# Optimization experiments

Measured on AMD Instinct MI355X. Metric: run time of the kernel, lower is better.

## Reference

```python
import jax, jax.numpy as jnp
import numpy as np

EPS = 1e-5  # torch BatchNorm default

def _conv(x, w, pad):
    return jax.lax.conv_general_dilated(x, w, window_strides=(1, 1), padding=pad,
                                        dimension_numbers=('NCHW', 'OIHW', 'NCHW'))

def _bn(x, g, b, m, v):
    # eval-mode BatchNorm2d over channel axis 1 of NCHW
    scale = g / jnp.sqrt(v + EPS)
    return x * scale[None, :, None, None] + (b - m * scale)[None, :, None, None]

def _bn1d(x, g, b, m, v):
    scale = g / jnp.sqrt(v + EPS)
    return x * scale[None, :] + (b - m * scale)[None, :]

def _prelu(x, a):
    # torch PReLU with num_parameters=1 (scalar slope, init 0.25)
    return jnp.where(x >= 0, x, a * x)

def setup_inputs():
    key = jax.random.key(0)
    ks = jax.random.split(key, 10)
    B, H, W = 256, 600, 19
    C1, C2 = 40, 40
    x = jax.random.normal(ks[0], (B, H, W), jnp.float32)
    w1 = jax.random.normal(ks[1], (C1, 1, 29, 1), jnp.float32) * 0.1
    w2 = jax.random.normal(ks[2], (C2, C1, 1, 19), jnp.float32) * 0.1
    fc1_w = jax.random.uniform(ks[3], (80, 1560), jnp.float32, -0.005, 0.005)
    fc2_w = jax.random.uniform(ks[4], (2, 80), jnp.float32, -0.005, 0.005)
    def bn_params(k, n):
        k1, k2 = jax.random.split(k)
        return (jnp.ones((n,), jnp.float32), jnp.zeros((n,), jnp.float32),
                jax.random.normal(k1, (n,), jnp.float32) * 0.1,
                jax.random.uniform(k2, (n,), jnp.float32, 0.5, 1.5))
    bn1_g, bn1_b, bn1_m, bn1_v = bn_params(ks[5], C1)
    bn2_g, bn2_b, bn2_m, bn2_v = bn_params(ks[6], C2)
    bn3_g, bn3_b, bn3_m, bn3_v = bn_params(ks[7], 80)
    a1 = jnp.full((1,), 0.25, jnp.float32)
    a2 = jnp.full((1,), 0.25, jnp.float32)
    a3 = jnp.full((1,), 0.25, jnp.float32)
    return dict(x=x, w1=w1, bn1_g=bn1_g, bn1_b=bn1_b, bn1_m=bn1_m, bn1_v=bn1_v, a1=a1,
                w2=w2, bn2_g=bn2_g, bn2_b=bn2_b, bn2_m=bn2_m, bn2_v=bn2_v, a2=a2,
                fc1_w=fc1_w, bn3_g=bn3_g, bn3_b=bn3_b, bn3_m=bn3_m, bn3_v=bn3_v, a3=a3,
                fc2_w=fc2_w)

def reference(x, w1, bn1_g, bn1_b, bn1_m, bn1_v, a1,
              w2, bn2_g, bn2_b, bn2_m, bn2_v, a2,
              fc1_w, bn3_g, bn3_b, bn3_m, bn3_v, a3, fc2_w):
    h = x[:, None, :, :]                                  # [B,1,600,19]
    # conv1: inputs NOT binarized, weights sign-binarized
    h = _conv(h, jnp.sign(w1), [(14, 14), (0, 0)])         # [B,40,600,19]
    h = _prelu(_bn(h, bn1_g, bn1_b, bn1_m, bn1_v), a1)
    # conv2: inputs and weights binarized
    h = _conv(jnp.sign(h), jnp.sign(w2), [(0, 0), (0, 0)])  # [B,40,600,1]
    h = _prelu(_bn(h, bn2_g, bn2_b, bn2_m, bn2_v), a2)
    # AvgPool2d kernel (30,1) stride (15,1)
    h = jax.lax.reduce_window(h, 0.0, jax.lax.add, (1, 1, 30, 1), (1, 1, 15, 1), 'VALID') / 30.0  # [B,40,39,1]
    h = h.reshape(h.shape[0], -1)                          # [B,1560]
    # fc1: binarized input/weight; BatchNorm1d; PReLU; dropout is identity in eval
    h = jnp.sign(h) @ jnp.sign(fc1_w).T                    # [B,80]
    h = _prelu(_bn1d(h, bn3_g, bn3_b, bn3_m, bn3_v), a3)
    out = jnp.sign(h) @ jnp.sign(fc2_w).T                  # [B,2]
    return out
```

## Files before the change

kernel.cpp:

```cpp
#include <hip/hip_runtime.h>
#include <stdint.h>

#define B_ 256
#define H_ 600
#define W_ 19
#define C1_ 40
#define C2_ 40
#define KH_ 29
#define PAD_ 14
#define NW_ 760
#define NWORDS_ 12
#define NJ_ 39
#define FIN_ 1560
#define FOUT_ 80
#define FCW_ 25
#define HS1 150
#define XSTL 179

__device__ __forceinline__ float fsgn(float x){ return (x > 0.f) ? 1.f : ((x < 0.f) ? -1.f : 0.f); }
__device__ __forceinline__ int8_t isgn(float x){ return (int8_t)((x > 0.f) - (x < 0.f)); }

__global__ void k0_setup(const float* __restrict__ w1, const float* __restrict__ w2,
                         const float* __restrict__ fc1w, const float* __restrict__ fc2w,
                         const float* __restrict__ g1, const float* __restrict__ b1,
                         const float* __restrict__ m1, const float* __restrict__ v1,
                         const float* __restrict__ g2, const float* __restrict__ b2,
                         const float* __restrict__ m2, const float* __restrict__ v2,
                         const float* __restrict__ g3, const float* __restrict__ b3,
                         const float* __restrict__ m3, const float* __restrict__ v3,
                         float* __restrict__ w1s, uint64_t* __restrict__ w2m,
                         uint64_t* __restrict__ fc1p, int8_t* __restrict__ fc2s,
                         float* __restrict__ bnp)
{
  int tid = blockIdx.x * blockDim.x + threadIdx.x;
  int np  = gridDim.x * blockDim.x;
  int lane = threadIdx.x & 63;
  int gw   = tid >> 6;
  int nw   = np >> 6;

  for (int i = tid; i < C1_*KH_; i += np) w1s[i] = fsgn(w1[i]);

  for (int v = gw; v < C2_*NWORDS_; v += nw){
    int c2 = v / NWORDS_, wd = v % NWORDS_;
    int idx = wd*64 + lane;
    float val = 0.f;
    if (idx < NW_){
      int c1 = idx % 40, w = idx / 40;
      val = w2[c2*NW_ + c1*W_ + w];
    }
    unsigned long long m = __ballot(val > 0.f);
    if (lane == 0) w2m[c2*NWORDS_ + wd] = m;
  }
  for (int v = gw; v < FOUT_*2*FCW_; v += nw){
    int o = v / (2*FCW_), r = v % (2*FCW_);
    int neg = r / FCW_, wd = r % FCW_;
    int e = wd*64 + lane;
    float val = (e < FIN_) ? fc1w[o*FIN_ + e] : 0.f;
    unsigned long long m = __ballot(neg ? (val < 0.f) : (val > 0.f));
    if (lane == 0) fc1p[o*(2*FCW_) + r] = m;
  }
  for (int i = tid; i < 2*FOUT_; i += np) fc2s[i] = isgn(fc2w[i]);
  for (int i = tid; i < C1_; i += np){
    float s = __fdiv_rn(g1[i], __fsqrt_rn(__fadd_rn(v1[i], 1e-5f)));
    bnp[i] = s; bnp[40+i] = __fsub_rn(b1[i], __fmul_rn(m1[i], s));
  }
  for (int i = tid; i < C2_; i += np){
    float s = __fdiv_rn(g2[i], __fsqrt_rn(__fadd_rn(v2[i], 1e-5f)));
    bnp[80+i] = s; bnp[120+i] = __fsub_rn(b2[i], __fmul_rn(m2[i], s));
  }
  for (int i = tid; i < FOUT_; i += np){
    float s = __fdiv_rn(g3[i], __fsqrt_rn(__fadd_rn(v3[i], 1e-5f)));
    bnp[160+i] = s; bnp[240+i] = __fsub_rn(b3[i], __fmul_rn(m3[i], s));
  }
}

__device__ __forceinline__ float opaque(float v){ asm volatile("" : "+v"(v)); return v; }

template<int T>
__device__ __forceinline__ float acc29(float (&xw)[29], float (&wt)[29]){
  float a = 0.f;
  #pragma unroll
  for (int k = 0; k < 29; ++k)
    a = __builtin_fmaf(wt[k], xw[(T + k) % 29], a);
  return a;
}

template<int T>
__device__ __forceinline__ void step1(float (&xw)[29], float (&wt)[29],
                                      const float* xck, ulonglong2* ob,
                                      float scale, float bias, int lane){
  xw[(T + 28) % 29] = opaque(xck[T + 28]);
  float acc = acc29<T>(xw, wt);
  float z = __fadd_rn(__fmul_rn(acc, scale), bias);
  unsigned long long pp = __ballot(z > 0.f);
  unsigned long long nn = __ballot(z < 0.f);
  if (lane == 0){ ulonglong2 v; v.x = pp; v.y = pp | nn; ob[T] = v; }
}

#define S1(t) step1<t>(xw, wt, xck, ob, scale, bias, lane);

__global__ __launch_bounds__(256, 6) void k1_conv1(const float* __restrict__ x,
                                                   const float* __restrict__ w1s,
                                                   const float* __restrict__ bnp,
                                                   uint64_t* __restrict__ s1bits)
{
  __shared__ float xs[W_ * XSTL];
  int b = blockIdx.x, ht = blockIdx.y, g = blockIdx.z;
  int h0 = HS1 * ht;
  const float* xb = x + (size_t)b * H_ * W_;
  for (int i = threadIdx.x; i < (HS1 + 28) * W_; i += 256){
    int r = i / W_, w = i % W_;
    int gh = h0 - PAD_ + r;
    xs[w*XSTL + r] = (gh >= 0 && gh < H_) ? xb[gh*W_ + w] : 0.f;
  }
  __syncthreads();

  int lane = threadIdx.x & 63, wave = threadIdx.x >> 6;
  int wd   = g*4 + wave;
  int idx  = wd*64 + lane;
  bool valid = (idx < NW_);
  int c1 = idx % 40;
  int w  = valid ? (idx / 40) : 18;

  float wt[KH_];
  #pragma unroll
  for (int k = 0; k < KH_; ++k) wt[k] = opaque(w1s[c1*KH_ + k]);
  float scale = bnp[c1], bias = bnp[40 + c1];
  if (!valid){ scale = __builtin_nanf(""); bias = scale; }
  const float* xcol = &xs[w * XSTL];

  float xw[29];
  #pragma unroll
  for (int s = 0; s < 28; ++s) xw[s] = opaque(xcol[s]);

  ulonglong2* obase = (ulonglong2*)s1bits + ((size_t)(b*12 + wd) * H_ + h0);

  #pragma unroll 1
  for (int c = 0; c < 5; ++c){
    const float* xck = xcol + 29*c;
    ulonglong2* ob = obase + 29*c;
    S1(0)  S1(1)  S1(2)  S1(3)  S1(4)  S1(5)  S1(6)  S1(7)  S1(8)  S1(9)
    S1(10) S1(11) S1(12) S1(13) S1(14) S1(15) S1(16) S1(17) S1(18) S1(19)
    S1(20) S1(21) S1(22) S1(23) S1(24) S1(25) S1(26) S1(27) S1(28)
  }
  {
    const float* xck = xcol + 145;
    ulonglong2* ob = obase + 145;
    S1(0) S1(1) S1(2) S1(3) S1(4)
  }
}

__global__ __launch_bounds__(640) void k2_fused(const uint64_t* __restrict__ s1bits,
                                                const uint64_t* __restrict__ w2m_g,
                                                const uint64_t* __restrict__ fc1p,
                                                const int8_t* __restrict__ fc2s,
                                                const float* __restrict__ bnp,
                                                const float* __restrict__ a2p,
                                                const float* __restrict__ a3p,
                                                float* __restrict__ out)
{
  __shared__ float z[C2_][640];
  __shared__ uint64_t spP[FCW_], spN[FCW_];
  __shared__ int z3[FOUT_];
  int b = blockIdx.x;
  int tid = threadIdx.x;
  int lane = tid & 63;
  int rowc = (tid < H_) ? tid : (H_ - 1);

  uint64_t Pv[NWORDS_], Mv[NWORDS_];
  const ulonglong2* sb = (const ulonglong2*)s1bits + (size_t)b * NWORDS_ * H_;
  #pragma unroll
  for (int wd = 0; wd < NWORDS_; ++wd){
    ulonglong2 pm = sb[(size_t)wd * H_ + rowc];
    Pv[wd] = pm.x; Mv[wd] = pm.y;
  }
  int nzv = 0;
  #pragma unroll
  for (int wd = 0; wd < NWORDS_; ++wd) nzv += __popcll(Mv[wd]);

  float alpha2 = a2p[0];
  #pragma unroll 2
  for (int c2 = 0; c2 < C2_; ++c2){
    int dsum = 0;
    #pragma unroll
    for (int wd = 0; wd < NWORDS_; ++wd)
      dsum += __popcll(Mv[wd] & (Pv[wd] ^ w2m_g[c2*NWORDS_ + wd]));
    int y = nzv - 2*dsum;
    float u = __fadd_rn(__fmul_rn((float)y, bnp[80 + c2]), bnp[120 + c2]);
    z[c2][tid] = (u >= 0.f) ? u : __fmul_rn(alpha2, u);
  }
  __syncthreads();

  #pragma unroll 1
  for (int ch = 0; ch < 3; ++ch){
    int o = ch*640 + tid;
    bool act = (o < FIN_);
    int c2 = act ? (o / NJ_) : 0, j = act ? (o % NJ_) : 0;
    int base = 15*j;
    float s = 0.f;
    #pragma unroll
    for (int r = 0; r < 30; ++r) s = __fadd_rn(s, z[c2][base + r]);
    unsigned long long pp = __ballot(act && (s > 0.f));
    unsigned long long nn = __ballot(act && (s < 0.f));
    int word = ch*10 + (tid >> 6);
    if (lane == 0 && word < FCW_){ spP[word] = pp; spN[word] = nn; }
  }
  __syncthreads();

  float alpha3 = a3p[0];
  if (tid < FOUT_){
    int o = tid;
    const uint64_t* wp = fc1p + o * (2*FCW_);
    int acc = 0;
    #pragma unroll
    for (int wd = 0; wd < FCW_; ++wd){
      uint64_t P = spP[wd], N = spN[wd];
      uint64_t WP = wp[wd], WN = wp[FCW_ + wd];
      acc += __popcll(P & WP) + __popcll(N & WN) - __popcll(P & WN) - __popcll(N & WP);
    }
    float u = __fadd_rn(__fmul_rn((float)acc, bnp[160 + o]), bnp[240 + o]);
    float zz = (u >= 0.f) ? u : __fmul_rn(alpha3, u);
    z3[o] = (zz > 0.f) - (zz < 0.f);
  }
  __syncthreads();
  if (tid < 2){
    int acc = 0;
    for (int o = 0; o < FOUT_; ++o) acc += z3[o] * (int)fc2s[tid * FOUT_ + o];
    out[b*2 + tid] = (float)acc;
  }
}

extern "C" void kernel_launch(void* const* d_in, const int* in_sizes, int n_in,
                              void* d_out, int out_size, void* d_ws, size_t ws_size,
                              hipStream_t stream)
{
  const float* x    = (const float*)d_in[0];
  const float* w1   = (const float*)d_in[1];
  const float* g1   = (const float*)d_in[2];
  const float* b1   = (const float*)d_in[3];
  const float* m1   = (const float*)d_in[4];
  const float* v1   = (const float*)d_in[5];
  const float* a1   = (const float*)d_in[6];   (void)a1;
  const float* w2   = (const float*)d_in[7];
  const float* g2   = (const float*)d_in[8];
  const float* b2   = (const float*)d_in[9];
  const float* m2   = (const float*)d_in[10];
  const float* v2   = (const float*)d_in[11];
  const float* a2   = (const float*)d_in[12];
  const float* fc1w = (const float*)d_in[13];
  const float* g3   = (const float*)d_in[14];
  const float* b3   = (const float*)d_in[15];
  const float* m3   = (const float*)d_in[16];
  const float* v3   = (const float*)d_in[17];
  const float* a3   = (const float*)d_in[18];
  const float* fc2w = (const float*)d_in[19];

  char* ws = (char*)d_ws;
  uint64_t* s1bits = (uint64_t*)(ws);
  uint64_t* w2m    = (uint64_t*)(ws + 29491200);
  float*    w1s    = (float*)   (ws + 29495040);
  float*    bnp    = (float*)   (ws + 29499680);
  uint64_t* fc1p   = (uint64_t*)(ws + 29500960);
  int8_t*   fc2s   = (int8_t*)  (ws + 29532960);

  k0_setup<<<dim3(128), dim3(256), 0, stream>>>(w1, w2, fc1w, fc2w,
                                                g1, b1, m1, v1,
                                                g2, b2, m2, v2,
                                                g3, b3, m3, v3,
                                                w1s, w2m, fc1p, fc2s, bnp);
  k1_conv1<<<dim3(B_, 4, 3), dim3(256), 0, stream>>>(x, w1s, bnp, s1bits);
  k2_fused<<<dim3(B_), dim3(640), 0, stream>>>(s1bits, w2m, fc1p, fc2s, bnp,
                                               a2, a3, (float*)d_out);
}
```

Before: 220.9 us.

## Fuse all stages into one cooperative persistent kernel with grid syncs

Replaces the three kernel launches with a single cooperative kernel of 512 blocks that runs setup, conv1, conv2/pool and the FC layers in phases separated by grid-wide syncs. Conv1 now computes four output rows per thread from vectorised shared-memory loads. Conv2 is split across two blocks per batch, each handling half the channels, with the pooled signs passed through global memory. This is meant to remove launch gaps and improve conv1 register reuse, at the cost of grid-sync overhead and much lower parallelism, since only 512 blocks of 256 threads each cover the conv1 work.

```diff
diff --git a/kernel.cpp b/kernel.cpp
--- a/kernel.cpp
+++ b/kernel.cpp
@@ -1,4 +1,5 @@
 #include <hip/hip_runtime.h>
+#include <hip/hip_cooperative_groups.h>
 #include <stdint.h>
 
 #define B_ 256
@@ -14,219 +15,219 @@
 #define FIN_ 1560
 #define FOUT_ 80
 #define FCW_ 25
-#define HS1 150
-#define XSTL 179
-
-__device__ __forceinline__ float fsgn(float x){ return (x > 0.f) ? 1.f : ((x < 0.f) ? -1.f : 0.f); }
-__device__ __forceinline__ int8_t isgn(float x){ return (int8_t)((x > 0.f) - (x < 0.f)); }
-
-__global__ void k0_setup(const float* __restrict__ w1, const float* __restrict__ w2,
-                         const float* __restrict__ fc1w, const float* __restrict__ fc2w,
-                         const float* __restrict__ g1, const float* __restrict__ b1,
-                         const float* __restrict__ m1, const float* __restrict__ v1,
-                         const float* __restrict__ g2, const float* __restrict__ b2,
-                         const float* __restrict__ m2, const float* __restrict__ v2,
-                         const float* __restrict__ g3, const float* __restrict__ b3,
-                         const float* __restrict__ m3, const float* __restrict__ v3,
-                         float* __restrict__ w1s, uint64_t* __restrict__ w2m,
-                         uint64_t* __restrict__ fc1p, int8_t* __restrict__ fc2s,
-                         float* __restrict__ bnp)
+#define HS1 300
+#define XSTL2 332
+
+typedef float vf4 __attribute__((ext_vector_type(4)));
+
+struct Pargs {
+  const float *x,*w1,*g1,*b1,*m1,*v1,*w2,*g2,*b2,*m2,*v2,*a2,
+              *fc1w,*g3,*b3,*m3,*v3,*a3,*fc2w;
+  float *w1s,*bnp,*out;
+  uint64_t *w2m,*fc1p,*s1b;
+  int8_t *fc2s,*sp;
+};
+
+union alignas(16) SharedU {
+  float xs[W_ * XSTL2];
+  struct { float z[20][601]; uint64_t w2l[20][NWORDS_]; float bnl[80]; } p2;
+  struct { uint64_t spP[FCW_], spN[FCW_]; int z3[FOUT_]; } p3;
+};
+
+__global__ __launch_bounds__(256, 2) void fused(Pargs P)
 {
-  int tid = blockIdx.x * blockDim.x + threadIdx.x;
-  int np  = gridDim.x * blockDim.x;
-  int lane = threadIdx.x & 63;
-  int gw   = tid >> 6;
-  int nw   = np >> 6;
-
-  for (int i = tid; i < C1_*KH_; i += np) w1s[i] = fsgn(w1[i]);
-
-  for (int v = gw; v < C2_*NWORDS_; v += nw){
-    int c2 = v / NWORDS_, wd = v % NWORDS_;
-    int idx = wd*64 + lane;
-    float val = 0.f;
-    if (idx < NW_){
-      int c1 = idx % 40, w = idx / 40;
-      val = w2[c2*NW_ + c1*W_ + w];
-    }
-    unsigned long long m = __ballot(val > 0.f);
-    if (lane == 0) w2m[c2*NWORDS_ + wd] = m;
-  }
-  for (int v = gw; v < FOUT_*2*FCW_; v += nw){
-    int o = v / (2*FCW_), r = v % (2*FCW_);
-    int neg = r / FCW_, wd = r % FCW_;
-    int e = wd*64 + lane;
-    float val = (e < FIN_) ? fc1w[o*FIN_ + e] : 0.f;
-    unsigned long long m = __ballot(neg ? (val < 0.f) : (val > 0.f));
-    if (lane == 0) fc1p[o*(2*FCW_) + r] = m;
-  }
-  for (int i = tid; i < 2*FOUT_; i += np) fc2s[i] = isgn(fc2w[i]);
-  for (int i = tid; i < C1_; i += np){
-    float s = __fdiv_rn(g1[i], __fsqrt_rn(__fadd_rn(v1[i], 1e-5f)));
-    bnp[i] = s; bnp[40+i] = __fsub_rn(b1[i], __fmul_rn(m1[i], s));
-  }
-  for (int i = tid; i < C2_; i += np){
-    float s = __fdiv_rn(g2[i], __fsqrt_rn(__fadd_rn(v2[i], 1e-5f)));
-    bnp[80+i] = s; bnp[120+i] = __fsub_rn(b2[i], __fmul_rn(m2[i], s));
-  }
-  for (int i = tid; i < FOUT_; i += np){
-    float s = __fdiv_rn(g3[i], __fsqrt_rn(__fadd_rn(v3[i], 1e-5f)));
-    bnp[160+i] = s; bnp[240+i] = __fsub_rn(b3[i], __fmul_rn(m3[i], s));
-  }
-}
-
-__device__ __forceinline__ float opaque(float v){ asm volatile("" : "+v"(v)); return v; }
-
-template<int T>
-__device__ __forceinline__ float acc29(float (&xw)[29], float (&wt)[29]){
-  float a = 0.f;
-  #pragma unroll
-  for (int k = 0; k < 29; ++k)
-    a = __builtin_fmaf(wt[k], xw[(T + k) % 29], a);
-  return a;
-}
-
-template<int T>
-__device__ __forceinline__ void step1(float (&xw)[29], float (&wt)[29],
-                                      const float* xck, ulonglong2* ob,
-                                      float scale, float bias, int lane){
-  xw[(T + 28) % 29] = opaque(xck[T + 28]);
-  float acc = acc29<T>(xw, wt);
-  float z = __fadd_rn(__fmul_rn(acc, scale), bias);
-  unsigned long long pp = __ballot(z > 0.f);
-  unsigned long long nn = __ballot(z < 0.f);
-  if (lane == 0){ ulonglong2 v; v.x = pp; v.y = pp | nn; ob[T] = v; }
-}
-
-#define S1(t) step1<t>(xw, wt, xck, ob, scale, bias, lane);
-
-__global__ __launch_bounds__(256, 6) void k1_conv1(const float* __restrict__ x,
-                                                   const float* __restrict__ w1s,
-                                                   const float* __restrict__ bnp,
-                                                   uint64_t* __restrict__ s1bits)
-{
-  __shared__ float xs[W_ * XSTL];
-  int b = blockIdx.x, ht = blockIdx.y, g = blockIdx.z;
-  int h0 = HS1 * ht;
-  const float* xb = x + (size_t)b * H_ * W_;
-  for (int i = threadIdx.x; i < (HS1 + 28) * W_; i += 256){
-    int r = i / W_, w = i % W_;
-    int gh = h0 - PAD_ + r;
-    xs[w*XSTL + r] = (gh >= 0 && gh < H_) ? xb[gh*W_ + w] : 0.f;
-  }
-  __syncthreads();
-
-  int lane = threadIdx.x & 63, wave = threadIdx.x >> 6;
-  int wd   = g*4 + wave;
-  int idx  = wd*64 + lane;
-  bool valid = (idx < NW_);
-  int c1 = idx % 40;
-  int w  = valid ? (idx / 40) : 18;
-
-  float wt[KH_];
-  #pragma unroll
-  for (int k = 0; k < KH_; ++k) wt[k] = opaque(w1s[c1*KH_ + k]);
-  float scale = bnp[c1], bias = bnp[40 + c1];
-  if (!valid){ scale = __builtin_nanf(""); bias = scale; }
-  const float* xcol = &xs[w * XSTL];
-
-  float xw[29];
-  #pragma unroll
-  for (int s = 0; s < 28; ++s) xw[s] = opaque(xcol[s]);
-
-  ulonglong2* obase = (ulonglong2*)s1bits + ((size_t)(b*12 + wd) * H_ + h0);
-
-  #pragma unroll 1
-  for (int c = 0; c < 5; ++c){
-    const float* xck = xcol + 29*c;
-    ulonglong2* ob = obase + 29*c;
-    S1(0)  S1(1)  S1(2)  S1(3)  S1(4)  S1(5)  S1(6)  S1(7)  S1(8)  S1(9)
-    S1(10) S1(11) S1(12) S1(13) S1(14) S1(15) S1(16) S1(17) S1(18) S1(19)
-    S1(20) S1(21) S1(22) S1(23) S1(24) S1(25) S1(26) S1(27) S1(28)
-  }
+  cooperative_groups::grid_group grid = cooperative_groups::this_grid();
+  __shared__ SharedU sh;
+  const int bid = blockIdx.x, tid = threadIdx.x;
+  const int lane = tid & 63, wave = tid >> 6;
+
   {
-    const float* xck = xcol + 145;
-    ulonglong2* ob = obase + 145;
-    S1(0) S1(1) S1(2) S1(3) S1(4)
-  }
-}
-
-__global__ __launch_bounds__(640) void k2_fused(const uint64_t* __restrict__ s1bits,
-                                                const uint64_t* __restrict__ w2m_g,
-                                                const uint64_t* __restrict__ fc1p,
-                                                const int8_t* __restrict__ fc2s,
-                                                const float* __restrict__ bnp,
-                                                const float* __restrict__ a2p,
-                                                const float* __restrict__ a3p,
-                                                float* __restrict__ out)
-{
-  __shared__ float z[C2_][640];
-  __shared__ uint64_t spP[FCW_], spN[FCW_];
-  __shared__ int z3[FOUT_];
-  int b = blockIdx.x;
-  int tid = threadIdx.x;
-  int lane = tid & 63;
-  int rowc = (tid < H_) ? tid : (H_ - 1);
-
-  uint64_t Pv[NWORDS_], Mv[NWORDS_];
-  const ulonglong2* sb = (const ulonglong2*)s1bits + (size_t)b * NWORDS_ * H_;
-  #pragma unroll
-  for (int wd = 0; wd < NWORDS_; ++wd){
-    ulonglong2 pm = sb[(size_t)wd * H_ + rowc];
-    Pv[wd] = pm.x; Mv[wd] = pm.y;
-  }
-  int nzv = 0;
-  #pragma unroll
-  for (int wd = 0; wd < NWORDS_; ++wd) nzv += __popcll(Mv[wd]);
-
-  float alpha2 = a2p[0];
-  #pragma unroll 2
-  for (int c2 = 0; c2 < C2_; ++c2){
-    int dsum = 0;
-    #pragma unroll
-    for (int wd = 0; wd < NWORDS_; ++wd)
-      dsum += __popcll(Mv[wd] & (Pv[wd] ^ w2m_g[c2*NWORDS_ + wd]));
-    int y = nzv - 2*dsum;
-    float u = __fadd_rn(__fmul_rn((float)y, bnp[80 + c2]), bnp[120 + c2]);
-    z[c2][tid] = (u >= 0.f) ? u : __fmul_rn(alpha2, u);
-  }
-  __syncthreads();
-
-  #pragma unroll 1
-  for (int ch = 0; ch < 3; ++ch){
-    int o = ch*640 + tid;
-    bool act = (o < FIN_);
-    int c2 = act ? (o / NJ_) : 0, j = act ? (o % NJ_) : 0;
-    int base = 15*j;
-    float s = 0.f;
-    #pragma unroll
-    for (int r = 0; r < 30; ++r) s = __fadd_rn(s, z[c2][base + r]);
-    unsigned long long pp = __ballot(act && (s > 0.f));
-    unsigned long long nn = __ballot(act && (s < 0.f));
-    int word = ch*10 + (tid >> 6);
-    if (lane == 0 && word < FCW_){ spP[word] = pp; spN[word] = nn; }
-  }
-  __syncthreads();
-
-  float alpha3 = a3p[0];
-  if (tid < FOUT_){
-    int o = tid;
-    const uint64_t* wp = fc1p + o * (2*FCW_);
-    int acc = 0;
-    #pragma unroll
-    for (int wd = 0; wd < FCW_; ++wd){
-      uint64_t P = spP[wd], N = spN[wd];
-      uint64_t WP = wp[wd], WN = wp[FCW_ + wd];
-      acc += __popcll(P & WP) + __popcll(N & WN) - __popcll(P & WN) - __popcll(N & WP);
-    }
-    float u = __fadd_rn(__fmul_rn((float)acc, bnp[160 + o]), bnp[240 + o]);
-    float zz = (u >= 0.f) ? u : __fmul_rn(alpha3, u);
-    z3[o] = (zz > 0.f) - (zz < 0.f);
-  }
-  __syncthreads();
-  if (tid < 2){
-    int acc = 0;
-    for (int o = 0; o < FOUT_; ++o) acc += z3[o] * (int)fc2s[tid * FOUT_ + o];
-    out[b*2 + tid] = (float)acc;
+    int t0 = bid*256 + tid, np = 512*256;
+    int gw = bid*4 + wave,  nw = 512*4;
+    for (int i = t0; i < C1_*KH_; i += np){
+      float v = P.w1[i];
+      P.w1s[i] = (v > 0.f) ? 1.f : ((v < 0.f) ? -1.f : 0.f);
+    }
+    for (int v = gw; v < C2_*NWORDS_; v += nw){
+      int c2 = v / NWORDS_, wd = v % NWORDS_;
+      int idx = wd*64 + lane;
+      float val = 0.f;
+      if (idx < NW_){ int c1 = idx % 40, w = idx / 40; val = P.w2[c2*NW_ + c1*W_ + w]; }
+      unsigned long long m = __ballot(val > 0.f);
+      if (lane == 0) P.w2m[c2*NWORDS_ + wd] = m;
+    }
+    for (int v = gw; v < FOUT_*2*FCW_; v += nw){
+      int o = v / (2*FCW_), r = v % (2*FCW_);
+      int neg = r / FCW_, wd = r % FCW_;
+      int e = wd*64 + lane;
+      float val = (e < FIN_) ? P.fc1w[o*FIN_ + e] : 0.f;
+      unsigned long long m = __ballot(neg ? (val < 0.f) : (val > 0.f));
+      if (lane == 0) P.fc1p[o*(2*FCW_) + r] = m;
+    }
+    for (int i = t0; i < 2*FOUT_; i += np){
+      float v = P.fc2w[i]; P.fc2s[i] = (int8_t)((v > 0.f) - (v < 0.f));
+    }
+    for (int i = t0; i < C1_; i += np){
+      float s = __fdiv_rn(P.g1[i], __fsqrt_rn(__fadd_rn(P.v1[i], 1e-5f)));
+      P.bnp[i] = s; P.bnp[40+i] = __fsub_rn(P.b1[i], __fmul_rn(P.m1[i], s));
+    }
+    for (int i = t0; i < C2_; i += np){
+      float s = __fdiv_rn(P.g2[i], __fsqrt_rn(__fadd_rn(P.v2[i], 1e-5f)));
+      P.bnp[80+i] = s; P.bnp[120+i] = __fsub_rn(P.b2[i], __fmul_rn(P.m2[i], s));
+    }
+    for (int i = t0; i < FOUT_; i += np){
+      float s = __fdiv_rn(P.g3[i], __fsqrt_rn(__fadd_rn(P.v3[i], 1e-5f)));
+      P.bnp[160+i] = s; P.bnp[240+i] = __fsub_rn(P.b3[i], __fmul_rn(P.m3[i], s));
+    }
+  }
+  grid.sync();
+
+  {
+    int b = bid >> 1, ht = bid & 1;
+    int h0 = HS1 * ht;
+    const float* xb = P.x + (size_t)b * H_ * W_;
+    for (int i = tid; i < (HS1 + 28) * W_; i += 256){
+      int r = i / W_, w = i % W_;
+      int gh = h0 - PAD_ + r;
+      sh.xs[w*XSTL2 + r] = (gh >= 0 && gh < H_) ? xb[gh*W_ + w] : 0.f;
+    }
+    __syncthreads();
+
+    #pragma unroll 1
+    for (int rd = 0; rd < 3; ++rd){
+      int wd  = rd*4 + wave;
+      int idx = wd*64 + lane;
+      bool valid = (idx < NW_);
+      int c1 = idx % 40;
+      int w  = valid ? (idx / 40) : 18;
+
+      float wt[KH_];
+      #pragma unroll
+      for (int k = 0; k < KH_; ++k) wt[k] = P.w1s[c1*KH_ + k];
+      float scale = P.bnp[c1], bias = P.bnp[40 + c1];
+      if (!valid){ scale = __builtin_nanf(""); bias = scale; }
+      const float* xcol = &sh.xs[w * XSTL2];
+      ulonglong2* ob = (ulonglong2*)P.s1b + ((size_t)(b*12 + wd) * H_ + h0);
+
+      #pragma unroll 1
+      for (int n = 0; n < 75; ++n){
+        const vf4* xq = (const vf4*)xcol + n;
+        vf4 q0=xq[0],q1=xq[1],q2=xq[2],q3=xq[3],q4=xq[4],q5=xq[5],q6=xq[6],q7=xq[7];
+        asm volatile("" : "+v"(q0),"+v"(q1),"+v"(q2),"+v"(q3),
+                          "+v"(q4),"+v"(q5),"+v"(q6),"+v"(q7));
+        float xv[32];
+        #pragma unroll
+        for (int j = 0; j < 4; ++j){
+          xv[j]=q0[j]; xv[4+j]=q1[j]; xv[8+j]=q2[j];  xv[12+j]=q3[j];
+          xv[16+j]=q4[j]; xv[20+j]=q5[j]; xv[24+j]=q6[j]; xv[28+j]=q7[j];
+        }
+        float a0=0.f, a1=0.f, a2=0.f, a3=0.f;
+        #pragma unroll
+        for (int k = 0; k < 29; ++k){
+          float wk = wt[k];
+          a0 = __builtin_fmaf(wk, xv[k],   a0);
+          a1 = __builtin_fmaf(wk, xv[k+1], a1);
+          a2 = __builtin_fmaf(wk, xv[k+2], a2);
+          a3 = __builtin_fmaf(wk, xv[k+3], a3);
+        }
+        float z0 = __fadd_rn(__fmul_rn(a0, scale), bias);
+        float z1 = __fadd_rn(__fmul_rn(a1, scale), bias);
+        float z2 = __fadd_rn(__fmul_rn(a2, scale), bias);
+        float z3 = __fadd_rn(__fmul_rn(a3, scale), bias);
+        unsigned long long bp0=__ballot(z0>0.f), bm0=__ballot(z0<0.f);
+        unsigned long long bp1=__ballot(z1>0.f), bm1=__ballot(z1<0.f);
+        unsigned long long bp2=__ballot(z2>0.f), bm2=__ballot(z2<0.f);
+        unsigned long long bp3=__ballot(z3>0.f), bm3=__ballot(z3<0.f);
+        if (lane == 0){
+          ulonglong2 t;
+          t.x = bp0; t.y = bp0 | bm0; ob[4*n+0] = t;
+          t.x = bp1; t.y = bp1 | bm1; ob[4*n+1] = t;
+          t.x = bp2; t.y = bp2 | bm2; ob[4*n+2] = t;
+          t.x = bp3; t.y = bp3 | bm3; ob[4*n+3] = t;
+        }
+      }
+    }
+  }
+  grid.sync();
+
+  {
+    int b = bid >> 1, half = bid & 1;
+    for (int i = tid; i < 20*NWORDS_; i += 256)
+      ((uint64_t*)sh.p2.w2l)[i] = P.w2m[half*20*NWORDS_ + i];
+    for (int i = tid; i < 80; i += 256) sh.p2.bnl[i] = P.bnp[80 + i];
+    __syncthreads();
+
+    float alpha2 = P.a2[0];
+    const ulonglong2* sb = (const ulonglong2*)P.s1b + (size_t)b * NWORDS_ * H_;
+    #pragma unroll 1
+    for (int ps = 0; ps < 3; ++ps){
+      int row = ps*256 + tid;
+      if (row < H_){
+        uint64_t Pv[NWORDS_], Mv[NWORDS_];
+        #pragma unroll
+        for (int wd = 0; wd < NWORDS_; ++wd){
+          ulonglong2 pm = sb[(size_t)wd * H_ + row];
+          Pv[wd] = pm.x; Mv[wd] = pm.y;
+        }
+        int nzv = 0;
+        #pragma unroll
+        for (int wd = 0; wd < NWORDS_; ++wd) nzv += __popcll(Mv[wd]);
+        #pragma unroll 2
+        for (int cl = 0; cl < 20; ++cl){
+          int c2 = half*20 + cl;
+          int dsum = 0;
+          #pragma unroll
+          for (int wd = 0; wd < NWORDS_; ++wd)
+            dsum += __popcll(Mv[wd] & (Pv[wd] ^ sh.p2.w2l[cl][wd]));
+          int y = nzv - 2*dsum;
+          float u = __fadd_rn(__fmul_rn((float)y, sh.p2.bnl[c2]), sh.p2.bnl[40 + c2]);
+          sh.p2.z[cl][row] = (u >= 0.f) ? u : __fmul_rn(alpha2, u);
+        }
+      }
+    }
+    __syncthreads();
+    for (int o = tid; o < 20*NJ_; o += 256){
+      int cl = o / NJ_, j = o % NJ_;
+      int base = 15*j;
+      float s = 0.f;
+      #pragma unroll
+      for (int r = 0; r < 30; ++r) s = __fadd_rn(s, sh.p2.z[cl][base + r]);
+      P.sp[(size_t)b*FIN_ + (half*20 + cl)*NJ_ + j] = (int8_t)((s > 0.f) - (s < 0.f));
+    }
+  }
+  grid.sync();
+
+  if (bid < B_){
+    int b = bid;
+    const int8_t* spb = P.sp + (size_t)b * FIN_;
+    for (int wd = wave; wd < FCW_; wd += 4){
+      int e = wd*64 + lane;
+      int v = (e < FIN_) ? (int)spb[e] : 0;
+      unsigned long long pp = __ballot(v > 0);
+      unsigned long long nn = __ballot(v < 0);
+      if (lane == 0){ sh.p3.spP[wd] = pp; sh.p3.spN[wd] = nn; }
+    }
+    __syncthreads();
+    float alpha3 = P.a3[0];
+    if (tid < FOUT_){
+      const uint64_t* wp = P.fc1p + tid * (2*FCW_);
+      int acc = 0;
+      #pragma unroll
+      for (int wd = 0; wd < FCW_; ++wd){
+        uint64_t Pp = sh.p3.spP[wd], Nn = sh.p3.spN[wd];
+        acc += __popcll(Pp & wp[wd]) + __popcll(Nn & wp[FCW_ + wd])
+             - __popcll(Pp & wp[FCW_ + wd]) - __popcll(Nn & wp[wd]);
+      }
+      float u = __fadd_rn(__fmul_rn((float)acc, P.bnp[160 + tid]), P.bnp[240 + tid]);
+      float zz = (u >= 0.f) ? u : __fmul_rn(alpha3, u);
+      sh.p3.z3[tid] = (zz > 0.f) - (zz < 0.f);
+    }
+    __syncthreads();
+    if (tid < 2){
+      int acc = 0;
+      for (int o = 0; o < FOUT_; ++o) acc += sh.p3.z3[o] * (int)P.fc2s[tid*FOUT_ + o];
+      P.out[b*2 + tid] = (float)acc;
+    }
   }
 }
 
@@ -234,41 +235,38 @@
                               void* d_out, int out_size, void* d_ws, size_t ws_size,
                               hipStream_t stream)
 {
-  const float* x    = (const float*)d_in[0];
-  const float* w1   = (const float*)d_in[1];
-  const float* g1   = (const float*)d_in[2];
-  const float* b1   = (const float*)d_in[3];
-  const float* m1   = (const float*)d_in[4];
-  const float* v1   = (const float*)d_in[5];
-  const float* a1   = (const float*)d_in[6];   (void)a1;
-  const float* w2   = (const float*)d_in[7];
-  const float* g2   = (const float*)d_in[8];
-  const float* b2   = (const float*)d_in[9];
-  const float* m2   = (const float*)d_in[10];
-  const float* v2   = (const float*)d_in[11];
-  const float* a2   = (const float*)d_in[12];
-  const float* fc1w = (const float*)d_in[13];
-  const float* g3   = (const float*)d_in[14];
-  const float* b3   = (const float*)d_in[15];
-  const float* m3   = (const float*)d_in[16];
-  const float* v3   = (const float*)d_in[17];
-  const float* a3   = (const float*)d_in[18];
-  const float* fc2w = (const float*)d_in[19];
-
   char* ws = (char*)d_ws;
-  uint64_t* s1bits = (uint64_t*)(ws);
-  uint64_t* w2m    = (uint64_t*)(ws + 29491200);
-  float*    w1s    = (float*)   (ws + 29495040);
-  float*    bnp    = (float*)   (ws + 29499680);
-  uint64_t* fc1p   = (uint64_t*)(ws + 29500960);
-  int8_t*   fc2s   = (int8_t*)  (ws + 29532960);
-
-  k0_setup<<<dim3(128), dim3(256), 0, stream>>>(w1, w2, fc1w, fc2w,
-                                                g1, b1, m1, v1,
-                                                g2, b2, m2, v2,
-                                                g3, b3, m3, v3,
-                                                w1s, w2m, fc1p, fc2s, bnp);
-  k1_conv1<<<dim3(B_, 4, 3), dim3(256), 0, stream>>>(x, w1s, bnp, s1bits);
-  k2_fused<<<dim3(B_), dim3(640), 0, stream>>>(s1bits, w2m, fc1p, fc2s, bnp,
-                                               a2, a3, (float*)d_out);
+  Pargs hp;
+  hp.x    = (const float*)d_in[0];
+  hp.w1   = (const float*)d_in[1];
+  hp.g1   = (const float*)d_in[2];
+  hp.b1   = (const float*)d_in[3];
+  hp.m1   = (const float*)d_in[4];
+  hp.v1   = (const float*)d_in[5];
+  hp.w2   = (const float*)d_in[7];
+  hp.g2   = (const float*)d_in[8];
+  hp.b2   = (const float*)d_in[9];
+  hp.m2   = (const float*)d_in[10];
+  hp.v2   = (const float*)d_in[11];
+  hp.a2   = (const float*)d_in[12];
+  hp.fc1w = (const float*)d_in[13];
+  hp.g3   = (const float*)d_in[14];
+  hp.b3   = (const float*)d_in[15];
+  hp.m3   = (const float*)d_in[16];
+  hp.v3   = (const float*)d_in[17];
+  hp.a3   = (const float*)d_in[18];
+  hp.fc2w = (const float*)d_in[19];
+
+  hp.s1b  = (uint64_t*)(ws);
+  hp.w2m  = (uint64_t*)(ws + 29491200);
+  hp.w1s  = (float*)   (ws + 29495040);
+  hp.bnp  = (float*)   (ws + 29499680);
+  hp.fc1p = (uint64_t*)(ws + 29500960);
+  hp.fc2s = (int8_t*)  (ws + 29532960);
+  hp.sp   = (int8_t*)  (ws + 29533120);
+  hp.out  = (float*)d_out;
+
+  void* args[] = { &hp };
+  hipLaunchCooperativeKernel(reinterpret_cast<void*>(fused),
+                             dim3(512), dim3(256), args, 0, stream);
 }
```

New measurement: 429.4 us. 1.94x slower.
